# Kernel tuning notes

Hardware: AMD Instinct MI355X
Metric: run time of the kernel (lower is better)

The kernel has to match this reference:

```python
import jax, jax.numpy as jnp
import numpy as np

PATCH = 7            # args.corr_size (local correlation window)
R = PATCH // 2       # displacement radius


def _disps():
    return [(dy, dx) for dy in range(PATCH) for dx in range(PATCH)]


def setup_inputs() -> dict:
    key = jax.random.key(0)
    k1, k2, k3 = jax.random.split(key, 3)
    B, De, Do, T, H, W = 4, 64, 64, 4, 128, 128
    m_in = jax.random.normal(k1, (B, De, T, H, W), jnp.float32)
    m_out = jax.random.normal(k2, (B, Do, T, H, W), jnp.float32)
    q_in = jax.random.normal(k3, (B, De, H, W), jnp.float32)
    const = jnp.zeros((1,), jnp.float32)  # learnable constant (init 0)
    return {"m_in": m_in, "m_out": m_out, "q_in": q_in, "const": const}


def reference(m_in, m_out, q_in, const):
    B, De, T, H, W = m_in.shape
    Do = m_out.shape[1]
    P2 = PATCH * PATCH
    # --- functionCorrelation over all T frames at once ---
    # p[b, d, t, h, w] = sum_c q[b,c,h,w] * m_in[b,c,t,h+dy-R,w+dx-R]  (zero-padded)
    mp = jnp.pad(m_in, ((0, 0), (0, 0), (0, 0), (R, R), (R, R)))
    p = jnp.stack(
        [jnp.einsum('bchw,bcthw->bthw', q_in, mp[:, :, :, dy:dy + H, dx:dx + W])
         for dy, dx in _disps()],
        axis=1)  # [B, P2, T, H, W]  (matches torch stack(dim=2) then disp at dim=1)
    # --- softmax over stacked (P2*T [+1 const]) channels ---
    logits = p.reshape(B, P2 * T, H, W)
    cst = jnp.broadcast_to(const.reshape(1, 1, 1, 1), (B, 1, H, W))
    logits = jnp.concatenate([logits, cst], axis=1)
    attn = jax.nn.softmax(logits, axis=1)[:, :-1]  # drop constant channel
    attn = attn.reshape(B, P2, T, H, W)
    # --- functionCorrelationTranspose summed over T (attention read) ---
    # mem[b,c,h,w] = sum_{t,d} attn[b,d,t,h,w] * m_out[b,c,t,h+dy-R,w+dx-R]
    vp = jnp.pad(m_out, ((0, 0), (0, 0), (0, 0), (R, R), (R, R)))
    mem = jnp.zeros((B, Do, H, W), m_out.dtype)
    for d, (dy, dx) in enumerate(_disps()):
        mem = mem + jnp.einsum('bthw,bcthw->bchw', attn[:, d], vp[:, :, :, dy:dy + H, dx:dx + W])
    return mem, attn
```

## Files before the change

### kernel.cpp

```cpp
#include <hip/hip_runtime.h>

#define ATTN_OFF 4194304
#define WS_F4_COUNT 3407872ull

__global__ __launch_bounds__(256, 2) void k1_corr(
    const float* __restrict__ m_in, const float* __restrict__ q_in,
    float* __restrict__ out)
{
  const int p = blockIdx.x + (blockIdx.y << 2) + (blockIdx.z << 6);
  const int l = ((p & 7) << 7) + (p >> 3);
  const int bx = l & 3, by = (l >> 2) & 15, bz = l >> 6;

  const int b = bz >> 2, t = bz & 3;
  const int h0 = by * 8, w0 = bx * 32;
  const int tid = threadIdx.x;
  const int tx = tid & 31, ty = tid >> 5;
  const int h = h0 + ty, w = w0 + tx;

  __shared__ float m_s[14][42][4];
  float* const lds = &m_s[0][0][0];

  float acc[49];
#pragma unroll
  for (int d = 0; d < 49; ++d) acc[d] = 0.f;

  int goff0, goff1, goff2, loff0, loff1, loff2;
  float msk0, msk1, msk2;
  {
    const int i0 = tid;
    const int y0 = i0 / 38, x0 = i0 - 38 * y0;
    const int gy0 = h0 - 3 + y0, gx0 = w0 - 3 + x0;
    msk0 = (((unsigned)gy0 < 128u) && ((unsigned)gx0 < 128u)) ? 1.f : 0.f;
    const int gyc0 = gy0 < 0 ? 0 : (gy0 > 127 ? 127 : gy0);
    const int gxc0 = gx0 < 0 ? 0 : (gx0 > 127 ? 127 : gx0);
    goff0 = (gyc0 << 7) + gxc0;
    loff0 = (y0 * 42 + x0 + 1) << 2;

    const int i1 = tid + 256;
    const int y1 = i1 / 38, x1 = i1 - 38 * y1;
    const int gy1 = h0 - 3 + y1, gx1 = w0 - 3 + x1;
    msk1 = (((unsigned)gy1 < 128u) && ((unsigned)gx1 < 128u)) ? 1.f : 0.f;
    const int gyc1 = gy1 < 0 ? 0 : (gy1 > 127 ? 127 : gy1);
    const int gxc1 = gx1 < 0 ? 0 : (gx1 > 127 ? 127 : gx1);
    goff1 = (gyc1 << 7) + gxc1;
    loff1 = (y1 * 42 + x1 + 1) << 2;

    const int i2 = tid + 512;
    const int i2c = i2 < 532 ? i2 : 531;
    const int y2 = i2c / 38, x2 = i2c - 38 * y2;
    const int gy2 = h0 - 3 + y2, gx2 = w0 - 3 + x2;
    msk2 = (((unsigned)gy2 < 128u) && ((unsigned)gx2 < 128u)) ? 1.f : 0.f;
    const int gyc2 = gy2 < 0 ? 0 : (gy2 > 127 ? 127 : gy2);
    const int gxc2 = gx2 < 0 ? 0 : (gx2 > 127 ? 127 : gx2);
    goff2 = (gyc2 << 7) + gxc2;
    loff2 = (y2 * 42 + x2 + 1) << 2;
  }
  const bool has2 = (tid < 20);

  float4 r0, r1, r2;
  {
    const float* base = m_in + ((b * 256 + t) << 14);
    const float* p0 = base + goff0;
    r0.x = p0[0]; r0.y = p0[65536]; r0.z = p0[131072]; r0.w = p0[196608];
    const float* p1 = base + goff1;
    r1.x = p1[0]; r1.y = p1[65536]; r1.z = p1[131072]; r1.w = p1[196608];
    r2 = make_float4(0.f, 0.f, 0.f, 0.f);
    if (has2) {
      const float* p2 = base + goff2;
      r2.x = p2[0]; r2.y = p2[65536]; r2.z = p2[131072]; r2.w = p2[196608];
    }
  }

#pragma unroll 1
  for (int cc = 0; cc < 16; ++cc) {
    __syncthreads();
    *(float4*)(lds + loff0) = make_float4(r0.x*msk0, r0.y*msk0, r0.z*msk0, r0.w*msk0);
    *(float4*)(lds + loff1) = make_float4(r1.x*msk1, r1.y*msk1, r1.z*msk1, r1.w*msk1);
    if (has2)
      *(float4*)(lds + loff2) = make_float4(r2.x*msk2, r2.y*msk2, r2.z*msk2, r2.w*msk2);
    __syncthreads();

    if (cc < 15) {
      const float* base = m_in + (((b * 64 + (cc + 1) * 4) * 4 + t) << 14);
      const float* p0 = base + goff0;
      r0.x = p0[0]; r0.y = p0[65536]; r0.z = p0[131072]; r0.w = p0[196608];
      const float* p1 = base + goff1;
      r1.x = p1[0]; r1.y = p1[65536]; r1.z = p1[131072]; r1.w = p1[196608];
      if (has2) {
        const float* p2 = base + goff2;
        r2.x = p2[0]; r2.y = p2[65536]; r2.z = p2[131072]; r2.w = p2[196608];
      }
    }

    float q0[4];
#pragma unroll
    for (int k = 0; k < 4; ++k)
      q0[k] = q_in[((b * 64 + cc * 4 + k) << 14) + (h << 7) + w];
#pragma unroll
    for (int dy = 0; dy < 7; ++dy)
#pragma unroll
      for (int dx = 0; dx < 7; ++dx) {
        const float4 mv = *(const float4*)&m_s[ty + dy][tx + 1 + dx][0];
        acc[dy * 7 + dx] += q0[0]*mv.x + q0[1]*mv.y + q0[2]*mv.z + q0[3]*mv.w;
      }
  }

  const int obase = ATTN_OFF + ((b * 196 + t) << 14) + (h << 7) + w;
#pragma unroll
  for (int d = 0; d < 49; ++d)
    out[obase + ((d * 4) << 14)] = acc[d];
}

__global__ __launch_bounds__(256) void k2_softmax(
    float* __restrict__ out, const float* __restrict__ cst,
    float4* __restrict__ ws)
{
  const int tid = threadIdx.x;
  const int pl = tid & 63;
  const int t  = tid >> 6;
  const int pix = blockIdx.x * 64 + pl;
  const int b = pix >> 14, hw = pix & 16383;
  float* base = out + ATTN_OFF + ((b * 196 + t) << 14) + hw;

  float v[49];
#pragma unroll
  for (int d = 0; d < 49; ++d) v[d] = base[(d * 4) << 14];

  float mx = -1e30f;
#pragma unroll
  for (int d = 0; d < 49; ++d) mx = fmaxf(mx, v[d]);

  __shared__ float red[4][64];
  red[t][pl] = mx;
  __syncthreads();
  float M = fmaxf(fmaxf(red[0][pl], red[1][pl]), fmaxf(red[2][pl], red[3][pl]));
  M = fmaxf(M, cst[0]);
  __syncthreads();

  float s = 0.f;
#pragma unroll
  for (int d = 0; d < 49; ++d) { v[d] = __expf(v[d] - M); s += v[d]; }
  red[t][pl] = s;
  __syncthreads();
  const float l = red[0][pl] + red[1][pl] + red[2][pl] + red[3][pl]
                + __expf(cst[0] - M);
  const float inv = 1.f / l;
#pragma unroll
  for (int d = 0; d < 49; ++d) {
    const float r = v[d] * inv;
    base[(d * 4) << 14] = r;
    v[d] = r;
  }

  if (ws) {
    const int h = hw >> 7, wc = hw & 127;
    const int G    = ((h >> 1) << 2) + (wc >> 5);
    const int lane = ((h & 1) << 5) + (wc & 31);
    float4* dst = ws + (size_t)(((b * 256 + G) * 4 + t) * 13) * 64 + lane;
#pragma unroll
    for (int g = 0; g < 13; ++g) {
      float4 p;
      p.x = v[g * 4];
      p.y = (g < 12) ? v[g * 4 + 1] : 0.f;
      p.z = (g < 12) ? v[g * 4 + 2] : 0.f;
      p.w = (g < 12) ? v[g * 4 + 3] : 0.f;
      dst[g * 64] = p;
    }
  }
}

__global__ __launch_bounds__(256) void k3_read_ws(
    const float* __restrict__ m_out, float* __restrict__ out,
    const float4* __restrict__ ws)
{
  const int p = blockIdx.x + (blockIdx.y << 2) + (blockIdx.z << 6);
  const int l = ((p & 7) << 8) + (p >> 3);
  const int cq = l & 7;
  const int tile = l >> 3;
  const int bx = tile & 3, by = (tile >> 2) & 15, b = tile >> 6;

  const int h0 = by * 8, w0 = bx * 32;
  const int tid = threadIdx.x;
  const int tx = tid & 31, ty = tid >> 5;
  const int h = h0 + ty, w = w0 + tx;
  const int waveid = tid >> 6, lane = tid & 63;
  const int G = ((h0 >> 1) + waveid) * 4 + bx;

  __shared__ float m_s[2][14][42][4];
  float* const lds = &m_s[0][0][0][0];

  float acc[8];
#pragma unroll
  for (int i = 0; i < 8; ++i) acc[i] = 0.f;

  int goff0, goff1, goff2, goff3, goff4;
  int loff0, loff1, loff2, loff3, loff4;
  float msk0, msk1, msk2, msk3, msk4;
#define K3_DECOMP(K, GO, LO, MS)                                           \
  {                                                                        \
    const int it  = (tid + (K << 8)) < 1064 ? (tid + (K << 8)) : 1063;     \
    const int qd  = it >= 532;                                             \
    const int rem = it - 532 * qd;                                         \
    const int yy  = rem / 38;                                              \
    const int xx  = rem - 38 * yy;                                         \
    const int gy  = h0 - 3 + yy, gx = w0 - 3 + xx;                         \
    MS = (((unsigned)gy < 128u) && ((unsigned)gx < 128u)) ? 1.f : 0.f;     \
    const int gyc = gy < 0 ? 0 : (gy > 127 ? 127 : gy);                    \
    const int gxc = gx < 0 ? 0 : (gx > 127 ? 127 : gx);                    \
    GO = (qd << 18) + (gyc << 7) + gxc;                                    \
    LO = (((qd * 14 + yy) * 42) + xx + 1) << 2;                            \
  }
  K3_DECOMP(0, goff0, loff0, msk0)
  K3_DECOMP(1, goff1, loff1, msk1)
  K3_DECOMP(2, goff2, loff2, msk2)
  K3_DECOMP(3, goff3, loff3, msk3)
  K3_DECOMP(4, goff4, loff4, msk4)
#undef K3_DECOMP
  const bool has4 = (tid < 40);

  float4 r0, r1, r2, r3, r4;
#define K3_LOAD(T)                                                         \
  {                                                                        \
    const float* base = m_out + (((b * 64 + cq * 8) * 4 + (T)) << 14);     \
    const float* q;                                                        \
    q = base + goff0; r0.x = q[0]; r0.y = q[65536]; r0.z = q[131072]; r0.w = q[196608]; \
    q = base + goff1; r1.x = q[0]; r1.y = q[65536]; r1.z = q[131072]; r1.w = q[196608]; \
    q = base + goff2; r2.x = q[0]; r2.y = q[65536]; r2.z = q[131072]; r2.w = q[196608]; \
    q = base + goff3; r3.x = q[0]; r3.y = q[65536]; r3.z = q[131072]; r3.w = q[196608]; \
    if (has4) { q = base + goff4;                                          \
      r4.x = q[0]; r4.y = q[65536]; r4.z = q[131072]; r4.w = q[196608]; }  \
  }
  r4 = make_float4(0.f, 0.f, 0.f, 0.f);
  K3_LOAD(0)

#pragma unroll 1
  for (int t = 0; t < 4; ++t) {
    const float4* ap = ws + (size_t)(((b * 256 + G) * 4 + t) * 13) * 64 + lane;

    __syncthreads();
    *(float4*)(lds + loff0) = make_float4(r0.x*msk0, r0.y*msk0, r0.z*msk0, r0.w*msk0);
    *(float4*)(lds + loff1) = make_float4(r1.x*msk1, r1.y*msk1, r1.z*msk1, r1.w*msk1);
    *(float4*)(lds + loff2) = make_float4(r2.x*msk2, r2.y*msk2, r2.z*msk2, r2.w*msk2);
    *(float4*)(lds + loff3) = make_float4(r3.x*msk3, r3.y*msk3, r3.z*msk3, r3.w*msk3);
    if (has4)
      *(float4*)(lds + loff4) = make_float4(r4.x*msk4, r4.y*msk4, r4.z*msk4, r4.w*msk4);
    __syncthreads();

    if (t < 3) K3_LOAD(t + 1)

    float4 cur = ap[0];
#pragma unroll
    for (int g = 0; g < 13; ++g) {
      float4 nxt = cur;
      if (g < 12) nxt = ap[(g + 1) * 64];
#pragma unroll
      for (int j = 0; j < 4; ++j) {
        const int d = g * 4 + j;
        if (d >= 49) break;
        const int dy = d / 7, dx = d % 7;
        const float av = (j == 0) ? cur.x : (j == 1) ? cur.y
                       : (j == 2) ? cur.z : cur.w;
#pragma unroll
        for (int q = 0; q < 2; ++q) {
          const float4 mv = *(const float4*)&m_s[q][ty + dy][tx + dx + 1][0];
          acc[q * 4 + 0] += av * mv.x;
          acc[q * 4 + 1] += av * mv.y;
          acc[q * 4 + 2] += av * mv.z;
          acc[q * 4 + 3] += av * mv.w;
        }
      }
      cur = nxt;
    }
  }
#undef K3_LOAD

#pragma unroll
  for (int q = 0; q < 2; ++q)
#pragma unroll
    for (int k = 0; k < 4; ++k)
      out[((b * 64 + cq * 8 + q * 4 + k) << 14) + (h << 7) + w] = acc[q * 4 + k];
}

__global__ __launch_bounds__(256) void k3_read_fb(
    const float* __restrict__ m_out, float* __restrict__ out)
{
  const int b = blockIdx.z >> 2, cq = blockIdx.z & 3;
  const int h0 = blockIdx.y * 8, w0 = blockIdx.x * 32;
  const int tid = threadIdx.x;
  const int tx = tid & 31, ty = tid >> 5;
  const int h = h0 + ty, w = w0 + tx;

  __shared__ float m_s[4][14][38][4];
  const float* __restrict__ attn = out + ATTN_OFF;

  float acc[16];
#pragma unroll
  for (int i = 0; i < 16; ++i) acc[i] = 0.f;

#pragma unroll 1
  for (int t = 0; t < 4; ++t) {
    float a[49];
#pragma unroll
    for (int d = 0; d < 49; ++d)
      a[d] = attn[((b * 196 + d * 4 + t) << 14) + (h << 7) + w];

    __syncthreads();
    for (int e = tid; e < 8512; e += 256) {
      int c16 = e / 532; int rem = e - c16 * 532;
      int y = rem / 38;  int x = rem - y * 38;
      int gy = h0 - 3 + y, gx = w0 - 3 + x;
      float v = 0.f;
      if (gy >= 0 && gy < 128 && gx >= 0 && gx < 128)
        v = m_out[(((b * 64 + cq * 16 + c16) * 4 + t) << 14) + (gy << 7) + gx];
      m_s[c16 >> 2][y][x][c16 & 3] = v;
    }
    __syncthreads();

#pragma unroll
    for (int dy = 0; dy < 7; ++dy)
#pragma unroll
      for (int dx = 0; dx < 7; ++dx) {
        const float av = a[dy * 7 + dx];
#pragma unroll
        for (int q = 0; q < 4; ++q) {
          const float4 mv = *(const float4*)&m_s[q][ty + dy][tx + dx][0];
          acc[q * 4 + 0] += av * mv.x;
          acc[q * 4 + 1] += av * mv.y;
          acc[q * 4 + 2] += av * mv.z;
          acc[q * 4 + 3] += av * mv.w;
        }
      }
  }

#pragma unroll
  for (int q = 0; q < 4; ++q)
#pragma unroll
    for (int k = 0; k < 4; ++k)
      out[((b * 64 + cq * 16 + q * 4 + k) << 14) + (h << 7) + w] = acc[q * 4 + k];
}

extern "C" void kernel_launch(void* const* d_in, const int* in_sizes, int n_in,
                              void* d_out, int out_size, void* d_ws, size_t ws_size,
                              hipStream_t stream) {
  const float* m_in  = (const float*)d_in[0];
  const float* m_out = (const float*)d_in[1];
  const float* q_in  = (const float*)d_in[2];
  const float* cst   = (const float*)d_in[3];
  float* out = (float*)d_out;

  const bool use_ws = (ws_size >= WS_F4_COUNT * 16ull) && d_ws != nullptr;
  float4* ws = use_ws ? (float4*)d_ws : nullptr;

  k1_corr<<<dim3(4, 16, 16), dim3(256), 0, stream>>>(m_in, q_in, out);
  k2_softmax<<<dim3(1024), dim3(256), 0, stream>>>(out, cst, ws);
  if (use_ws)
    k3_read_ws<<<dim3(4, 16, 32), dim3(256), 0, stream>>>(m_out, out, ws);
  else
    k3_read_fb<<<dim3(4, 16, 16), dim3(256), 0, stream>>>(m_out, out);
}
```

Before: 130.6 us.

## Compute two output rows per thread in correlation kernel for LDS reuse

Each thread in the correlation kernel now computes two vertically adjacent output pixels, using a 16-row tile with a 22-row shared halo. Each LDS row read feeds both accumulators, which lowers LDS traffic and halo reload overhead per output. q_in loads for the next channel chunk are prefetched together with m_in. The cost is 98 accumulators per thread, so launch bounds drop to 1 block per CU and the grid is halved, which risks register pressure and lower occupancy.

```diff
diff --git a/kernel.cpp b/kernel.cpp
--- a/kernel.cpp
+++ b/kernel.cpp
@@ -3,72 +3,68 @@
 #define ATTN_OFF 4194304
 #define WS_F4_COUNT 3407872ull
 
-__global__ __launch_bounds__(256, 2) void k1_corr(
+__global__ __launch_bounds__(256, 1) void k1_corr(
     const float* __restrict__ m_in, const float* __restrict__ q_in,
     float* __restrict__ out)
 {
-  const int p = blockIdx.x + (blockIdx.y << 2) + (blockIdx.z << 6);
-  const int l = ((p & 7) << 7) + (p >> 3);
-  const int bx = l & 3, by = (l >> 2) & 15, bz = l >> 6;
+  const int p = blockIdx.x + (blockIdx.y << 2) + (blockIdx.z << 5);
+  const int l = ((p & 7) << 6) + (p >> 3);
+  const int bx = l & 3, by = (l >> 2) & 7, bz = l >> 5;
 
   const int b = bz >> 2, t = bz & 3;
-  const int h0 = by * 8, w0 = bx * 32;
+  const int h0 = by * 16, w0 = bx * 32;
   const int tid = threadIdx.x;
   const int tx = tid & 31, ty = tid >> 5;
-  const int h = h0 + ty, w = w0 + tx;
-
-  __shared__ float m_s[14][42][4];
+
+  __shared__ float m_s[22][42][4];
   float* const lds = &m_s[0][0][0];
 
-  float acc[49];
-#pragma unroll
-  for (int d = 0; d < 49; ++d) acc[d] = 0.f;
-
-  int goff0, goff1, goff2, loff0, loff1, loff2;
-  float msk0, msk1, msk2;
-  {
-    const int i0 = tid;
-    const int y0 = i0 / 38, x0 = i0 - 38 * y0;
-    const int gy0 = h0 - 3 + y0, gx0 = w0 - 3 + x0;
-    msk0 = (((unsigned)gy0 < 128u) && ((unsigned)gx0 < 128u)) ? 1.f : 0.f;
-    const int gyc0 = gy0 < 0 ? 0 : (gy0 > 127 ? 127 : gy0);
-    const int gxc0 = gx0 < 0 ? 0 : (gx0 > 127 ? 127 : gx0);
-    goff0 = (gyc0 << 7) + gxc0;
-    loff0 = (y0 * 42 + x0 + 1) << 2;
-
-    const int i1 = tid + 256;
-    const int y1 = i1 / 38, x1 = i1 - 38 * y1;
-    const int gy1 = h0 - 3 + y1, gx1 = w0 - 3 + x1;
-    msk1 = (((unsigned)gy1 < 128u) && ((unsigned)gx1 < 128u)) ? 1.f : 0.f;
-    const int gyc1 = gy1 < 0 ? 0 : (gy1 > 127 ? 127 : gy1);
-    const int gxc1 = gx1 < 0 ? 0 : (gx1 > 127 ? 127 : gx1);
-    goff1 = (gyc1 << 7) + gxc1;
-    loff1 = (y1 * 42 + x1 + 1) << 2;
-
-    const int i2 = tid + 512;
-    const int i2c = i2 < 532 ? i2 : 531;
-    const int y2 = i2c / 38, x2 = i2c - 38 * y2;
-    const int gy2 = h0 - 3 + y2, gx2 = w0 - 3 + x2;
-    msk2 = (((unsigned)gy2 < 128u) && ((unsigned)gx2 < 128u)) ? 1.f : 0.f;
-    const int gyc2 = gy2 < 0 ? 0 : (gy2 > 127 ? 127 : gy2);
-    const int gxc2 = gx2 < 0 ? 0 : (gx2 > 127 ? 127 : gx2);
-    goff2 = (gyc2 << 7) + gxc2;
-    loff2 = (y2 * 42 + x2 + 1) << 2;
-  }
-  const bool has2 = (tid < 20);
-
-  float4 r0, r1, r2;
-  {
-    const float* base = m_in + ((b * 256 + t) << 14);
-    const float* p0 = base + goff0;
-    r0.x = p0[0]; r0.y = p0[65536]; r0.z = p0[131072]; r0.w = p0[196608];
-    const float* p1 = base + goff1;
-    r1.x = p1[0]; r1.y = p1[65536]; r1.z = p1[131072]; r1.w = p1[196608];
-    r2 = make_float4(0.f, 0.f, 0.f, 0.f);
-    if (has2) {
-      const float* p2 = base + goff2;
-      r2.x = p2[0]; r2.y = p2[65536]; r2.z = p2[131072]; r2.w = p2[196608];
-    }
+  float acc0[49], acc1[49];
+#pragma unroll
+  for (int d = 0; d < 49; ++d) { acc0[d] = 0.f; acc1[d] = 0.f; }
+
+  int goff0, goff1, goff2, goff3, loff0, loff1, loff2, loff3;
+  float msk0, msk1, msk2, msk3;
+#define K1_DECOMP(K, GO, LO, MS)                                           \
+  {                                                                        \
+    const int it = (tid + (K << 8)) < 836 ? (tid + (K << 8)) : 835;        \
+    const int yy = it / 38;                                                \
+    const int xx = it - 38 * yy;                                           \
+    const int gy = h0 - 3 + yy, gx = w0 - 3 + xx;                          \
+    MS = (((unsigned)gy < 128u) && ((unsigned)gx < 128u)) ? 1.f : 0.f;     \
+    const int gyc = gy < 0 ? 0 : (gy > 127 ? 127 : gy);                    \
+    const int gxc = gx < 0 ? 0 : (gx > 127 ? 127 : gx);                    \
+    GO = (gyc << 7) + gxc;                                                 \
+    LO = (yy * 42 + xx + 1) << 2;                                          \
+  }
+  K1_DECOMP(0, goff0, loff0, msk0)
+  K1_DECOMP(1, goff1, loff1, msk1)
+  K1_DECOMP(2, goff2, loff2, msk2)
+  K1_DECOMP(3, goff3, loff3, msk3)
+#undef K1_DECOMP
+  const bool has3 = (tid < 68);
+
+  const int qpix = ((h0 + 2 * ty) << 7) + w0 + tx;
+
+  float4 r0, r1, r2, r3;
+  float qa[4], qb[4];
+#define K1_LOAD(CC)                                                        \
+  {                                                                        \
+    const float* base = m_in + (((b * 64 + (CC) * 4) * 4 + t) << 14);      \
+    const float* q;                                                        \
+    q = base + goff0; r0.x = q[0]; r0.y = q[65536]; r0.z = q[131072]; r0.w = q[196608]; \
+    q = base + goff1; r1.x = q[0]; r1.y = q[65536]; r1.z = q[131072]; r1.w = q[196608]; \
+    q = base + goff2; r2.x = q[0]; r2.y = q[65536]; r2.z = q[131072]; r2.w = q[196608]; \
+    if (has3) { q = base + goff3;                                          \
+      r3.x = q[0]; r3.y = q[65536]; r3.z = q[131072]; r3.w = q[196608]; }  \
+  }
+  r3 = make_float4(0.f, 0.f, 0.f, 0.f);
+  K1_LOAD(0)
+#pragma unroll
+  for (int k = 0; k < 4; ++k) {
+    const float* qp = q_in + ((b * 64 + k) << 14) + qpix;
+    qa[k] = qp[0];
+    qb[k] = qp[128];
   }
 
 #pragma unroll 1
@@ -76,39 +72,49 @@
     __syncthreads();
     *(float4*)(lds + loff0) = make_float4(r0.x*msk0, r0.y*msk0, r0.z*msk0, r0.w*msk0);
     *(float4*)(lds + loff1) = make_float4(r1.x*msk1, r1.y*msk1, r1.z*msk1, r1.w*msk1);
-    if (has2)
-      *(float4*)(lds + loff2) = make_float4(r2.x*msk2, r2.y*msk2, r2.z*msk2, r2.w*msk2);
-    __syncthreads();
-
+    *(float4*)(lds + loff2) = make_float4(r2.x*msk2, r2.y*msk2, r2.z*msk2, r2.w*msk2);
+    if (has3)
+      *(float4*)(lds + loff3) = make_float4(r3.x*msk3, r3.y*msk3, r3.z*msk3, r3.w*msk3);
+    __syncthreads();
+
+    float qan[4], qbn[4];
     if (cc < 15) {
-      const float* base = m_in + (((b * 64 + (cc + 1) * 4) * 4 + t) << 14);
-      const float* p0 = base + goff0;
-      r0.x = p0[0]; r0.y = p0[65536]; r0.z = p0[131072]; r0.w = p0[196608];
-      const float* p1 = base + goff1;
-      r1.x = p1[0]; r1.y = p1[65536]; r1.z = p1[131072]; r1.w = p1[196608];
-      if (has2) {
-        const float* p2 = base + goff2;
-        r2.x = p2[0]; r2.y = p2[65536]; r2.z = p2[131072]; r2.w = p2[196608];
+      K1_LOAD(cc + 1)
+#pragma unroll
+      for (int k = 0; k < 4; ++k) {
+        const float* qp = q_in + ((b * 64 + (cc + 1) * 4 + k) << 14) + qpix;
+        qan[k] = qp[0];
+        qbn[k] = qp[128];
       }
     }
 
-    float q0[4];
-#pragma unroll
-    for (int k = 0; k < 4; ++k)
-      q0[k] = q_in[((b * 64 + cc * 4 + k) << 14) + (h << 7) + w];
-#pragma unroll
-    for (int dy = 0; dy < 7; ++dy)
+#pragma unroll
+    for (int wr = 0; wr < 8; ++wr) {
+      const float4* rowp = (const float4*)&m_s[2 * ty + wr][tx + 1][0];
 #pragma unroll
       for (int dx = 0; dx < 7; ++dx) {
-        const float4 mv = *(const float4*)&m_s[ty + dy][tx + 1 + dx][0];
-        acc[dy * 7 + dx] += q0[0]*mv.x + q0[1]*mv.y + q0[2]*mv.z + q0[3]*mv.w;
+        const float4 mv = rowp[dx];
+        if (wr < 7)
+          acc0[wr * 7 + dx] += qa[0]*mv.x + qa[1]*mv.y + qa[2]*mv.z + qa[3]*mv.w;
+        if (wr > 0)
+          acc1[(wr - 1) * 7 + dx] += qb[0]*mv.x + qb[1]*mv.y + qb[2]*mv.z + qb[3]*mv.w;
       }
-  }
-
-  const int obase = ATTN_OFF + ((b * 196 + t) << 14) + (h << 7) + w;
-#pragma unroll
-  for (int d = 0; d < 49; ++d)
-    out[obase + ((d * 4) << 14)] = acc[d];
+    }
+
+    if (cc < 15) {
+#pragma unroll
+      for (int k = 0; k < 4; ++k) { qa[k] = qan[k]; qb[k] = qbn[k]; }
+    }
+  }
+#undef K1_LOAD
+
+  const int obase = ATTN_OFF + ((b * 196 + t) << 14)
+                  + ((h0 + 2 * ty) << 7) + w0 + tx;
+#pragma unroll
+  for (int d = 0; d < 49; ++d) {
+    out[obase +       ((d * 4) << 14)] = acc0[d];
+    out[obase + 128 + ((d * 4) << 14)] = acc1[d];
+  }
 }
 
 __global__ __launch_bounds__(256) void k2_softmax(
@@ -351,7 +357,7 @@
   const bool use_ws = (ws_size >= WS_F4_COUNT * 16ull) && d_ws != nullptr;
   float4* ws = use_ws ? (float4*)d_ws : nullptr;
 
-  k1_corr<<<dim3(4, 16, 16), dim3(256), 0, stream>>>(m_in, q_in, out);
+  k1_corr<<<dim3(4, 8, 16), dim3(256), 0, stream>>>(m_in, q_in, out);
   k2_softmax<<<dim3(1024), dim3(256), 0, stream>>>(out, cst, ws);
   if (use_ws)
     k3_read_ws<<<dim3(4, 16, 32), dim3(256), 0, stream>>>(m_out, out, ws);
```

After: 124.2 us, median of 2. 4.9% less time.
